# Optimization experiments

Measured on AMD Instinct MI355X. Metric: run time of the kernel, lower is better.

Reference implementation:

```python
import jax, jax.numpy as jnp
import numpy as np

B, C, T = 64, 1, 262144
NUM_BANDS = 6
# (min, max) for each of the 18 normalized control params: 6 bands x (gain_dB, cutoff_Hz, Q)
PARAM_RANGES = np.array([
    [-24.0, 24.0], [20.0, 200.0], [0.1, 10.0],      # low shelf
    [-24.0, 24.0], [200.0, 2000.0], [0.1, 10.0],    # band 1
    [-24.0, 24.0], [200.0, 2000.0], [0.1, 10.0],    # band 2
    [-24.0, 24.0], [2000.0, 8000.0], [0.1, 10.0],   # band 3
    [-24.0, 24.0], [4000.0, 12000.0], [0.1, 10.0],  # band 4
    [-24.0, 24.0], [4000.0, 12000.0], [0.1, 10.0],  # high shelf
], dtype=np.float32)
FILTER_TYPES = ["low_shelf", "peaking", "peaking", "peaking", "peaking", "high_shelf"]


def biquad_coeffs(gain_dB, cutoff, q, sr, ftype):
    # Audio-EQ-cookbook biquad coefficients; all inputs shape (B,)
    A = 10.0 ** (gain_dB / 40.0)
    w0 = 2.0 * jnp.pi * (cutoff / sr)
    alpha = jnp.sin(w0) / (2.0 * q)
    c = jnp.cos(w0)
    sA = jnp.sqrt(A)
    if ftype == "low_shelf":
        b0 = A * ((A + 1) - (A - 1) * c + 2 * sA * alpha)
        b1 = 2 * A * ((A - 1) - (A + 1) * c)
        b2 = A * ((A + 1) - (A - 1) * c - 2 * sA * alpha)
        a0 = (A + 1) + (A - 1) * c + 2 * sA * alpha
        a1 = -2 * ((A - 1) + (A + 1) * c)
        a2 = (A + 1) + (A - 1) * c - 2 * sA * alpha
    elif ftype == "high_shelf":
        b0 = A * ((A + 1) + (A - 1) * c + 2 * sA * alpha)
        b1 = -2 * A * ((A - 1) + (A + 1) * c)
        b2 = A * ((A + 1) + (A - 1) * c - 2 * sA * alpha)
        a0 = (A + 1) - (A - 1) * c + 2 * sA * alpha
        a1 = 2 * ((A - 1) - (A + 1) * c)
        a2 = (A + 1) - (A - 1) * c - 2 * sA * alpha
    else:  # peaking
        b0 = 1 + alpha * A
        b1 = -2 * c
        b2 = 1 - alpha * A
        a0 = 1 + alpha / A
        a1 = -2 * c
        a2 = 1 - alpha / A
    bcoef = jnp.stack([b0, b1, b2], axis=-1) / a0[..., None]  # (B, 3)
    acoef = jnp.stack([a0, a1, a2], axis=-1) / a0[..., None]  # (B, 3)
    return bcoef, acoef


def cascade_biquads(x, bcoefs, acoefs):
    # x: (N, T); bcoefs/acoefs: (6, N, 3). Fused cascade of 6 biquads,
    # direct form II transposed, single scan over time.
    def step(state, xt):  # state: (6, N, 2); xt: (N,)
        v = xt
        new_states = []
        for k in range(NUM_BANDS):
            bk, ak = bcoefs[k], acoefs[k]
            s1, s2 = state[k, :, 0], state[k, :, 1]
            y = bk[:, 0] * v + s1
            ns1 = bk[:, 1] * v - ak[:, 1] * y + s2
            ns2 = bk[:, 2] * v - ak[:, 2] * y
            new_states.append(jnp.stack([ns1, ns2], axis=-1))
            v = y
        return jnp.stack(new_states, axis=0), v
    init = jnp.zeros((NUM_BANDS, x.shape[0], 2), dtype=x.dtype)
    _, y = jax.lax.scan(step, init, x.T)  # y: (T, N)
    return y.T


def setup_inputs() -> dict:
    key = jax.random.key(0)
    k1, k2, k3 = jax.random.split(key, 3)
    x = jax.random.normal(k1, (B, C, T), dtype=jnp.float32) * 0.1
    p = jax.random.normal(k2, (B, 22), dtype=jnp.float32)
    W = jax.random.normal(k3, (18, 22), dtype=jnp.float32) * (1.0 / np.sqrt(22.0))
    b = jnp.zeros((18,), dtype=jnp.float32)
    return {"x": x, "p": p, "W": W, "b": b, "sample_rate": 24000}


def reference(x, p, W, b, sample_rate):
    bs, chs, s = x.shape
    sr = jnp.float32(sample_rate)
    # control path: linear + sigmoid -> 18 normalized params in [0, 1]
    pn = jax.nn.sigmoid(p @ W.T + b)  # (bs, 18)
    lo = jnp.asarray(PARAM_RANGES[:, 0])
    hi = jnp.asarray(PARAM_RANGES[:, 1])
    params = pn * (hi - lo) + lo  # denormalized, (bs, 18)
    bcoefs, acoefs = [], []
    for k, ftype in enumerate(FILTER_TYPES):
        g, f, q = params[:, 3 * k], params[:, 3 * k + 1], params[:, 3 * k + 2]
        bk, ak = biquad_coeffs(g, f, q, sr, ftype)
        bcoefs.append(bk)
        acoefs.append(ak)
    bcoefs = jnp.stack(bcoefs, axis=0)  # (6, bs, 3)
    acoefs = jnp.stack(acoefs, axis=0)
    # share each item's EQ across its channels
    bcoefs = jnp.repeat(bcoefs, chs, axis=1)  # (6, bs*chs, 3)
    acoefs = jnp.repeat(acoefs, chs, axis=1)
    y = cascade_biquads(x.reshape(bs * chs, s), bcoefs, acoefs)
    return y.reshape(bs, chs, s)
```

## Files before the change

### kernel.cpp

```cpp
#include <hip/hip_runtime.h>
#include <math.h>

#define NB    64
#define NT    262144
#define CH    64
#define NCK   (NT/CH)
#define NBANDS 6

#define COEF_OFF 0
#define MAT_OFF  4096
#define T_OFF    (MAT_OFF + NB*1728)
#define WPRE_OFF (T_OFF + NB*64*12)
#define D_OFF    (WPRE_OFF + NB*64*12)

struct Coef { float b0, b1, b2, a1, a2; };

__device__ __forceinline__ float rfl(float x) {
  return __int_as_float(__builtin_amdgcn_readfirstlane(__float_as_int(x)));
}

__device__ __forceinline__ float cascade_step(float v, float s[12], const Coef cf[NBANDS]) {
#pragma unroll
  for (int k = 0; k < NBANDS; ++k) {
    float s1 = s[2*k], s2 = s[2*k+1];
    float y   = fmaf(cf[k].b0, v, s1);
    float ns1 = fmaf(cf[k].b1, v, fmaf(-cf[k].a1, y, s2));
    float ns2 = fmaf(cf[k].b2, v, -cf[k].a2 * y);
    s[2*k]   = ns1;
    s[2*k+1] = ns2;
    v = y;
  }
  return v;
}

__device__ __forceinline__ void load_coefs(const float* ws, int batch, Coef cf[NBANDS]) {
  const float* c = ws + COEF_OFF + batch*30;
#pragma unroll
  for (int k = 0; k < NBANDS; ++k) {
    cf[k].b0 = rfl(c[5*k+0]); cf[k].b1 = rfl(c[5*k+1]); cf[k].b2 = rfl(c[5*k+2]);
    cf[k].a1 = rfl(c[5*k+3]); cf[k].a2 = rfl(c[5*k+4]);
  }
}

__global__ __launch_bounds__(64) void k_prep(const float* __restrict__ p, const float* __restrict__ W,
                                             const float* __restrict__ bias, const int* __restrict__ srp,
                                             float* __restrict__ ws) {
  __shared__ float prmS[18];
  __shared__ float cfS[30];
  __shared__ float M0[144], M1[144];
  int b = blockIdx.x, tid = threadIdx.x;
  const float lo[18] = {-24.f,20.f,0.1f,  -24.f,200.f,0.1f,  -24.f,200.f,0.1f,
                        -24.f,2000.f,0.1f, -24.f,4000.f,0.1f, -24.f,4000.f,0.1f};
  const float hi[18] = { 24.f,200.f,10.f,  24.f,2000.f,10.f,  24.f,2000.f,10.f,
                         24.f,8000.f,10.f, 24.f,12000.f,10.f, 24.f,12000.f,10.f};
  if (tid < 18) {
    float acc = bias[tid];
    for (int j = 0; j < 22; ++j) acc = fmaf(W[tid*22+j], p[b*22+j], acc);
    float sg = 1.f / (1.f + expf(-acc));
    prmS[tid] = sg * (hi[tid] - lo[tid]) + lo[tid];
  }
  __syncthreads();
  if (tid < 6) {
    int k = tid;
    float g = prmS[3*k], f = prmS[3*k+1], q = prmS[3*k+2];
    float sr = (float)srp[0];
    float A  = powf(10.f, g * (1.f/40.f));
    float w0 = 6.28318530717958647692f * (f / sr);
    float al = sinf(w0) / (2.f*q);
    float c  = cosf(w0);
    float sA = sqrtf(A);
    float b0,b1,b2,a0,a1,a2;
    if (k == 0) {
      b0 = A*((A+1.f) - (A-1.f)*c + 2.f*sA*al);
      b1 = 2.f*A*((A-1.f) - (A+1.f)*c);
      b2 = A*((A+1.f) - (A-1.f)*c - 2.f*sA*al);
      a0 = (A+1.f) + (A-1.f)*c + 2.f*sA*al;
      a1 = -2.f*((A-1.f) + (A+1.f)*c);
      a2 = (A+1.f) + (A-1.f)*c - 2.f*sA*al;
    } else if (k == 5) {
      b0 = A*((A+1.f) + (A-1.f)*c + 2.f*sA*al);
      b1 = -2.f*A*((A-1.f) + (A+1.f)*c);
      b2 = A*((A+1.f) + (A-1.f)*c - 2.f*sA*al);
      a0 = (A+1.f) - (A-1.f)*c + 2.f*sA*al;
      a1 = 2.f*((A-1.f) - (A+1.f)*c);
      a2 = (A+1.f) - (A-1.f)*c - 2.f*sA*al;
    } else {
      b0 = 1.f + al*A;
      b1 = -2.f*c;
      b2 = 1.f - al*A;
      a0 = 1.f + al/A;
      a1 = -2.f*c;
      a2 = 1.f - al/A;
    }
    float inv = 1.f/a0;
    float* cws = ws + COEF_OFF + b*30;
    cws[5*k+0] = cfS[5*k+0] = b0*inv;
    cws[5*k+1] = cfS[5*k+1] = b1*inv;
    cws[5*k+2] = cfS[5*k+2] = b2*inv;
    cws[5*k+3] = cfS[5*k+3] = a1*inv;
    cws[5*k+4] = cfS[5*k+4] = a2*inv;
  }
  __syncthreads();

  Coef cf[NBANDS];
#pragma unroll
  for (int k = 0; k < NBANDS; ++k) {
    cf[k].b0 = cfS[5*k+0]; cf[k].b1 = cfS[5*k+1]; cf[k].b2 = cfS[5*k+2];
    cf[k].a1 = cfS[5*k+3]; cf[k].a2 = cfS[5*k+4];
  }
  if (tid < 12) {
    float s[12];
#pragma unroll
    for (int r = 0; r < 12; ++r) s[r] = (r == tid) ? 1.f : 0.f;
    cascade_step(0.f, s, cf);
#pragma unroll
    for (int r = 0; r < 12; ++r) M0[r*12 + tid] = s[r];
  }
  __syncthreads();

  float w[12];
#pragma unroll
  for (int r = 0; r < 12; ++r) w[r] = 0.f;
  cascade_step(1.f, w, cf);
  int e63 = 63 - tid;

  float* S = M0; float* D = M1;
  float* mout = ws + MAT_OFF + (size_t)b*1728;
  for (int q = 0; q < 6; ++q) {
    if ((e63 >> q) & 1) {
      float t[12];
#pragma unroll
      for (int r = 0; r < 12; ++r) {
        float acc = 0.f;
#pragma unroll
        for (int k = 0; k < 12; ++k) acc = fmaf(S[r*12+k], w[k], acc);
        t[r] = acc;
      }
#pragma unroll
      for (int r = 0; r < 12; ++r) w[r] = t[r];
    }
    for (int e = tid; e < 144; e += 64) {
      int r = e/12, c = e%12;
      float acc = 0.f;
#pragma unroll
      for (int k = 0; k < 12; ++k) acc = fmaf(S[r*12+k], S[k*12+c], acc);
      D[e] = acc;
    }
    __syncthreads();
    float* t = S; S = D; D = t;
  }
  {
    float* vout = ws + WPRE_OFF + (size_t)b*768;
#pragma unroll
    for (int r = 0; r < 12; ++r) vout[tid*12 + r] = w[r];
  }
  for (int e = tid; e < 144; e += 64) mout[e] = S[e];
  for (int l = 1; l < 12; ++l) {
    for (int e = tid; e < 144; e += 64) {
      int r = e/12, c = e%12;
      float acc = 0.f;
#pragma unroll
      for (int k = 0; k < 12; ++k) acc = fmaf(S[r*12+k], S[k*12+c], acc);
      D[e] = acc;
    }
    __syncthreads();
    float* t = S; S = D; D = t;
    for (int e = tid; e < 144; e += 64) mout[l*144 + e] = S[e];
  }
}

__global__ __launch_bounds__(256) void k_passA(const float* __restrict__ x,
                                               const float* __restrict__ Vt,
                                               float* __restrict__ ws) {
  __shared__ float KM[6][144];
  int tid = threadIdx.x, wib = tid >> 6, lane = tid & 63;
  int gw = blockIdx.x*4 + wib;
  int batch = gw >> 6, wv = gw & 63;
  int batch_b = blockIdx.x >> 4;

  const float* mb = ws + MAT_OFF + (size_t)batch_b*1728;
  for (int e = tid; e < 864; e += 256) KM[e/144][e%144] = mb[e];
  __syncthreads();

  const float4* xp = (const float4*)x + (size_t)batch*65536 + (size_t)wv*1024 + (size_t)lane*16;
  const float* Vb = Vt + (size_t)batch_b*768;

  float4 xv[16];
#pragma unroll
  for (int k = 0; k < 16; ++k) xv[k] = xp[k];

  float s[12];
#pragma unroll
  for (int r = 0; r < 12; ++r) s[r] = 0.f;

#pragma unroll
  for (int k = 0; k < 16; ++k) {
    const float* vr = Vb + k*48;
#pragma unroll
    for (int r = 0; r < 12; ++r) {
      float acc = s[r];
      acc = fmaf(vr[r],      xv[k].x, acc);
      acc = fmaf(vr[12 + r], xv[k].y, acc);
      acc = fmaf(vr[24 + r], xv[k].z, acc);
      acc = fmaf(vr[36 + r], xv[k].w, acc);
      s[r] = acc;
    }
  }

#pragma unroll
  for (int l = 0; l < 6; ++l) {
    const int pd = 1 << l;
    float nb[12];
#pragma unroll
    for (int r = 0; r < 12; ++r) nb[r] = __shfl_up(s[r], pd);
    if (lane >= pd) {
#pragma unroll
      for (int r = 0; r < 12; ++r) {
        float acc = s[r];
#pragma unroll
        for (int c = 0; c < 12; ++c) acc = fmaf(KM[l][r*12+c], nb[c], acc);
        s[r] = acc;
      }
    }
  }

  if (lane == 63) {
    float4* tp = (float4*)(ws + T_OFF + ((size_t)batch*64 + wv)*12);
    tp[0] = make_float4(s[0], s[1], s[2],  s[3]);
    tp[1] = make_float4(s[4], s[5], s[6],  s[7]);
    tp[2] = make_float4(s[8], s[9], s[10], s[11]);
  }

  float e[12];
#pragma unroll
  for (int r = 0; r < 12; ++r) e[r] = __shfl_up(s[r], 1);
  if (lane == 0) {
#pragma unroll
    for (int r = 0; r < 12; ++r) e[r] = 0.f;
  }
  int chunk = wv*64 + lane;
  float4* dp = (float4*)(ws + D_OFF + ((size_t)batch*NCK + chunk)*12);
  dp[0] = make_float4(e[0], e[1], e[2],  e[3]);
  dp[1] = make_float4(e[4], e[5], e[6],  e[7]);
  dp[2] = make_float4(e[8], e[9], e[10], e[11]);
}

__global__ __launch_bounds__(64) void k_scanW(float* __restrict__ ws) {
  __shared__ float WM[6][144];
  int b = blockIdx.x, lane = threadIdx.x;
  const float* mb = ws + MAT_OFF + (size_t)b*1728 + 864;
  for (int e = lane; e < 864; e += 64) WM[e/144][e%144] = mb[e];
  __syncthreads();

  const float4* tp = (const float4*)(ws + T_OFF + ((size_t)b*64 + lane)*12);
  float4 a0 = tp[0], a1 = tp[1], a2 = tp[2];
  float s[12] = {a0.x,a0.y,a0.z,a0.w, a1.x,a1.y,a1.z,a1.w, a2.x,a2.y,a2.z,a2.w};

#pragma unroll
  for (int l = 0; l < 6; ++l) {
    const int pd = 1 << l;
    float nb[12];
#pragma unroll
    for (int r = 0; r < 12; ++r) nb[r] = __shfl_up(s[r], pd);
    if (lane >= pd) {
#pragma unroll
      for (int r = 0; r < 12; ++r) {
        float acc = s[r];
#pragma unroll
        for (int c = 0; c < 12; ++c) acc = fmaf(WM[l][r*12+c], nb[c], acc);
        s[r] = acc;
      }
    }
  }
  float e[12];
#pragma unroll
  for (int r = 0; r < 12; ++r) e[r] = __shfl_up(s[r], 1);
  if (lane == 0) {
#pragma unroll
    for (int r = 0; r < 12; ++r) e[r] = 0.f;
  }
  float4* wp = (float4*)(ws + WPRE_OFF + ((size_t)b*64 + lane)*12);
  wp[0] = make_float4(e[0], e[1], e[2],  e[3]);
  wp[1] = make_float4(e[4], e[5], e[6],  e[7]);
  wp[2] = make_float4(e[8], e[9], e[10], e[11]);
}

__global__ __launch_bounds__(256) void k_passB(const float* __restrict__ x, const float* __restrict__ ws,
                                               float* __restrict__ out) {
  __shared__ float4 buf[4][2][256];
  __shared__ float KM[6][144];
  int tid = threadIdx.x, wib = tid >> 6, lane = tid & 63;
  int gw = blockIdx.x*4 + wib;
  int batch = gw >> 6, wv = gw & 63;
  int batch_b = blockIdx.x >> 4;

  const float* mb = ws + MAT_OFF + (size_t)batch_b*1728;
  for (int e = tid; e < 864; e += 256) KM[e/144][e%144] = mb[e];
  __syncthreads();

  const float4* x4 = (const float4*)x;
  float4* out4 = (float4*)out;
  size_t gbase4 = (size_t)batch*65536 + (size_t)wv*1024;
  int r2 = lane >> 2, c2 = lane & 3;
  float4* bufA = buf[wib][0];
  float4* bufB = buf[wib][1];

  float4 va[4], vb[4];
#pragma unroll
  for (int j = 0; j < 4; ++j) va[j] = x4[gbase4 + (size_t)(j*16 + r2)*16 + c2];

  Coef cf[NBANDS];
  load_coefs(ws, batch, cf);

  int chunk = wv*64 + lane;
  const float4* dp = (const float4*)(ws + D_OFF + ((size_t)batch*NCK + chunk)*12);
  float4 e0 = dp[0], e1 = dp[1], e2 = dp[2];
  const float4* wp = (const float4*)(ws + WPRE_OFF + ((size_t)batch*64 + wv)*12);
  float4 w0 = wp[0], w1 = wp[1], w2 = wp[2];
  float R[12] = {w0.x,w0.y,w0.z,w0.w, w1.x,w1.y,w1.z,w1.w, w2.x,w2.y,w2.z,w2.w};
#pragma unroll
  for (int l = 0; l < 6; ++l) {
    float t[12];
#pragma unroll
    for (int r = 0; r < 12; ++r) {
      float acc = 0.f;
#pragma unroll
      for (int c = 0; c < 12; ++c) acc = fmaf(KM[l][r*12+c], R[c], acc);
      t[r] = acc;
    }
    bool sel = (lane >> l) & 1;
#pragma unroll
    for (int r = 0; r < 12; ++r) R[r] = sel ? t[r] : R[r];
  }
  float s[12] = {e0.x+R[0], e0.y+R[1], e0.z+R[2],  e0.w+R[3],
                 e1.x+R[4], e1.y+R[5], e1.z+R[6],  e1.w+R[7],
                 e2.x+R[8], e2.y+R[9], e2.z+R[10], e2.w+R[11]};

#pragma unroll
  for (int j = 0; j < 4; ++j) bufA[c2*64 + j*16 + r2] = va[j];
  asm volatile("s_waitcnt lgkmcnt(0)" ::: "memory");

#pragma unroll
  for (int q = 0; q < 4; ++q) {
    float4* bp = (q & 1) ? bufB : bufA;
    float4* bn = (q & 1) ? bufA : bufB;
    float4* vr = (q & 1) ? va : vb;
    if (q < 3) {
#pragma unroll
      for (int j = 0; j < 4; ++j)
        vr[j] = x4[gbase4 + (size_t)(j*16 + r2)*16 + (q+1)*4 + c2];
    }
#pragma unroll
    for (int t = 0; t < 4; ++t) {
      float4 xv = bp[t*64 + lane];
      float4 yv;
      yv.x = cascade_step(xv.x, s, cf);
      yv.y = cascade_step(xv.y, s, cf);
      yv.z = cascade_step(xv.z, s, cf);
      yv.w = cascade_step(xv.w, s, cf);
      bp[t*64 + lane] = yv;
    }
    asm volatile("s_waitcnt lgkmcnt(0)" ::: "memory");
#pragma unroll
    for (int j = 0; j < 4; ++j) {
      float4 w = bp[c2*64 + j*16 + r2];
      out4[gbase4 + (size_t)(j*16 + r2)*16 + q*4 + c2] = w;
    }
    if (q < 3) {
#pragma unroll
      for (int j = 0; j < 4; ++j) bn[c2*64 + j*16 + r2] = vr[j];
      asm volatile("s_waitcnt lgkmcnt(0)" ::: "memory");
    }
  }
}

extern "C" void kernel_launch(void* const* d_in, const int* in_sizes, int n_in,
                              void* d_out, int out_size, void* d_ws, size_t ws_size,
                              hipStream_t stream) {
  const float* x    = (const float*)d_in[0];
  const float* p    = (const float*)d_in[1];
  const float* W    = (const float*)d_in[2];
  const float* bias = (const float*)d_in[3];
  const int*   sr   = (const int*)d_in[4];
  float* ws  = (float*)d_ws;
  float* out = (float*)d_out;

  int passBlocks = (NB * NCK) / 256;
  hipLaunchKernelGGL(k_prep,  dim3(NB),         dim3(64),  0, stream, p, W, bias, sr, ws);
  hipLaunchKernelGGL(k_passA, dim3(passBlocks), dim3(256), 0, stream, x, ws + WPRE_OFF, ws);
  hipLaunchKernelGGL(k_scanW, dim3(NB),         dim3(64),  0, stream, ws);
  hipLaunchKernelGGL(k_passB, dim3(passBlocks), dim3(256), 0, stream, x, ws, out);
}
```

Measured before the change: 97.58 us.

## Recompute chunk states in replay kernel, dropping scan kernel and state buffers

Removes the separate wave-level scan kernel and the per-chunk entry-state writes to workspace. The replay kernel now recomputes the chunk projections and the intra-wave scan from the x values it holds in registers. It also redoes the 64-wave totals scan redundantly in every wave to get its prefix. This cuts one launch and a large workspace write/read round trip, at the cost of duplicated matrix-vector work and more register pressure (16 float4 held per lane, launch bounds of 4).

```diff
diff --git a/kernel.cpp b/kernel.cpp
--- a/kernel.cpp
+++ b/kernel.cpp
@@ -10,8 +10,7 @@
 #define COEF_OFF 0
 #define MAT_OFF  4096
 #define T_OFF    (MAT_OFF + NB*1728)
-#define WPRE_OFF (T_OFF + NB*64*12)
-#define D_OFF    (WPRE_OFF + NB*64*12)
+#define V_OFF    (T_OFF + NB*64*12)
 
 struct Coef { float b0, b1, b2, a1, a2; };
 
@@ -150,7 +149,7 @@
     float* t = S; S = D; D = t;
   }
   {
-    float* vout = ws + WPRE_OFF + (size_t)b*768;
+    float* vout = ws + V_OFF + (size_t)b*768;
 #pragma unroll
     for (int r = 0; r < 12; ++r) vout[tid*12 + r] = w[r];
   }
@@ -169,9 +168,8 @@
   }
 }
 
-__global__ __launch_bounds__(256) void k_passA(const float* __restrict__ x,
-                                               const float* __restrict__ Vt,
-                                               float* __restrict__ ws) {
+__global__ __launch_bounds__(256, 4) void k_totals(const float* __restrict__ x,
+                                                   float* __restrict__ ws) {
   __shared__ float KM[6][144];
   int tid = threadIdx.x, wib = tid >> 6, lane = tid & 63;
   int gw = blockIdx.x*4 + wib;
@@ -182,17 +180,17 @@
   for (int e = tid; e < 864; e += 256) KM[e/144][e%144] = mb[e];
   __syncthreads();
 
-  const float4* xp = (const float4*)x + (size_t)batch*65536 + (size_t)wv*1024 + (size_t)lane*16;
-  const float* Vb = Vt + (size_t)batch_b*768;
+  const float4* x4 = (const float4*)x;
+  size_t gbase4 = (size_t)batch*65536 + (size_t)wv*1024 + (size_t)lane*16;
+  const float* Vb = ws + V_OFF + (size_t)batch_b*768;
 
   float4 xv[16];
 #pragma unroll
-  for (int k = 0; k < 16; ++k) xv[k] = xp[k];
+  for (int k = 0; k < 16; ++k) xv[k] = x4[gbase4 + k];
 
   float s[12];
 #pragma unroll
   for (int r = 0; r < 12; ++r) s[r] = 0.f;
-
 #pragma unroll
   for (int k = 0; k < 16; ++k) {
     const float* vr = Vb + k*48;
@@ -230,94 +228,109 @@
     tp[1] = make_float4(s[4], s[5], s[6],  s[7]);
     tp[2] = make_float4(s[8], s[9], s[10], s[11]);
   }
-
-  float e[12];
-#pragma unroll
-  for (int r = 0; r < 12; ++r) e[r] = __shfl_up(s[r], 1);
-  if (lane == 0) {
-#pragma unroll
-    for (int r = 0; r < 12; ++r) e[r] = 0.f;
-  }
-  int chunk = wv*64 + lane;
-  float4* dp = (float4*)(ws + D_OFF + ((size_t)batch*NCK + chunk)*12);
-  dp[0] = make_float4(e[0], e[1], e[2],  e[3]);
-  dp[1] = make_float4(e[4], e[5], e[6],  e[7]);
-  dp[2] = make_float4(e[8], e[9], e[10], e[11]);
-}
-
-__global__ __launch_bounds__(64) void k_scanW(float* __restrict__ ws) {
-  __shared__ float WM[6][144];
-  int b = blockIdx.x, lane = threadIdx.x;
-  const float* mb = ws + MAT_OFF + (size_t)b*1728 + 864;
-  for (int e = lane; e < 864; e += 64) WM[e/144][e%144] = mb[e];
-  __syncthreads();
-
-  const float4* tp = (const float4*)(ws + T_OFF + ((size_t)b*64 + lane)*12);
-  float4 a0 = tp[0], a1 = tp[1], a2 = tp[2];
-  float s[12] = {a0.x,a0.y,a0.z,a0.w, a1.x,a1.y,a1.z,a1.w, a2.x,a2.y,a2.z,a2.w};
-
-#pragma unroll
-  for (int l = 0; l < 6; ++l) {
-    const int pd = 1 << l;
-    float nb[12];
-#pragma unroll
-    for (int r = 0; r < 12; ++r) nb[r] = __shfl_up(s[r], pd);
-    if (lane >= pd) {
-#pragma unroll
-      for (int r = 0; r < 12; ++r) {
-        float acc = s[r];
-#pragma unroll
-        for (int c = 0; c < 12; ++c) acc = fmaf(WM[l][r*12+c], nb[c], acc);
-        s[r] = acc;
-      }
-    }
-  }
-  float e[12];
-#pragma unroll
-  for (int r = 0; r < 12; ++r) e[r] = __shfl_up(s[r], 1);
-  if (lane == 0) {
-#pragma unroll
-    for (int r = 0; r < 12; ++r) e[r] = 0.f;
-  }
-  float4* wp = (float4*)(ws + WPRE_OFF + ((size_t)b*64 + lane)*12);
-  wp[0] = make_float4(e[0], e[1], e[2],  e[3]);
-  wp[1] = make_float4(e[4], e[5], e[6],  e[7]);
-  wp[2] = make_float4(e[8], e[9], e[10], e[11]);
-}
-
-__global__ __launch_bounds__(256) void k_passB(const float* __restrict__ x, const float* __restrict__ ws,
-                                               float* __restrict__ out) {
-  __shared__ float4 buf[4][2][256];
-  __shared__ float KM[6][144];
+}
+
+__global__ __launch_bounds__(256, 4) void k_replay(const float* __restrict__ x,
+                                                   const float* __restrict__ ws,
+                                                   float* __restrict__ out) {
+  __shared__ float KM[12][144];
+  __shared__ float4 sbuf[4][256];
   int tid = threadIdx.x, wib = tid >> 6, lane = tid & 63;
   int gw = blockIdx.x*4 + wib;
   int batch = gw >> 6, wv = gw & 63;
   int batch_b = blockIdx.x >> 4;
 
   const float* mb = ws + MAT_OFF + (size_t)batch_b*1728;
-  for (int e = tid; e < 864; e += 256) KM[e/144][e%144] = mb[e];
+  for (int e = tid; e < 1728; e += 256) KM[e/144][e%144] = mb[e];
+
+  Coef cf[NBANDS];
+  load_coefs(ws, batch, cf);
   __syncthreads();
 
   const float4* x4 = (const float4*)x;
   float4* out4 = (float4*)out;
-  size_t gbase4 = (size_t)batch*65536 + (size_t)wv*1024;
-  int r2 = lane >> 2, c2 = lane & 3;
-  float4* bufA = buf[wib][0];
-  float4* bufB = buf[wib][1];
-
-  float4 va[4], vb[4];
-#pragma unroll
-  for (int j = 0; j < 4; ++j) va[j] = x4[gbase4 + (size_t)(j*16 + r2)*16 + c2];
-
-  Coef cf[NBANDS];
-  load_coefs(ws, batch, cf);
-
-  int chunk = wv*64 + lane;
-  const float4* dp = (const float4*)(ws + D_OFF + ((size_t)batch*NCK + chunk)*12);
-  float4 e0 = dp[0], e1 = dp[1], e2 = dp[2];
-  const float4* wp = (const float4*)(ws + WPRE_OFF + ((size_t)batch*64 + wv)*12);
-  float4 w0 = wp[0], w1 = wp[1], w2 = wp[2];
-  float R[12] = {w0.x,w0.y,w0.z,w0.w, w1.x,w1.y,w1.z,w1.w, w2.x,w2.y,w2.z,w2.w};
+  size_t wbase4 = (size_t)batch*65536 + (size_t)wv*1024;
+  size_t gbase4 = wbase4 + (size_t)lane*16;
+  const float* Vb = ws + V_OFF + (size_t)batch_b*768;
+
+  float4 xv[16];
+#pragma unroll
+  for (int k = 0; k < 16; ++k) xv[k] = x4[gbase4 + k];
+
+  float s[12];
+#pragma unroll
+  for (int r = 0; r < 12; ++r) s[r] = 0.f;
+#pragma unroll
+  for (int k = 0; k < 16; ++k) {
+    const float* vr = Vb + k*48;
+#pragma unroll
+    for (int r = 0; r < 12; ++r) {
+      float acc = s[r];
+      acc = fmaf(vr[r],      xv[k].x, acc);
+      acc = fmaf(vr[12 + r], xv[k].y, acc);
+      acc = fmaf(vr[24 + r], xv[k].z, acc);
+      acc = fmaf(vr[36 + r], xv[k].w, acc);
+      s[r] = acc;
+    }
+  }
+
+#pragma unroll
+  for (int l = 0; l < 6; ++l) {
+    const int pd = 1 << l;
+    float nb[12];
+#pragma unroll
+    for (int r = 0; r < 12; ++r) nb[r] = __shfl_up(s[r], pd);
+    if (lane >= pd) {
+#pragma unroll
+      for (int r = 0; r < 12; ++r) {
+        float acc = s[r];
+#pragma unroll
+        for (int c = 0; c < 12; ++c) acc = fmaf(KM[l][r*12+c], nb[c], acc);
+        s[r] = acc;
+      }
+    }
+  }
+
+  float ex[12];
+#pragma unroll
+  for (int r = 0; r < 12; ++r) ex[r] = __shfl_up(s[r], 1);
+  if (lane == 0) {
+#pragma unroll
+    for (int r = 0; r < 12; ++r) ex[r] = 0.f;
+  }
+
+  const float4* tp = (const float4*)(ws + T_OFF + ((size_t)batch*64 + lane)*12);
+  float4 t0 = tp[0], t1 = tp[1], t2 = tp[2];
+  float sc[12] = {t0.x,t0.y,t0.z,t0.w, t1.x,t1.y,t1.z,t1.w, t2.x,t2.y,t2.z,t2.w};
+#pragma unroll
+  for (int l = 0; l < 6; ++l) {
+    const int pd = 1 << l;
+    float nb[12];
+#pragma unroll
+    for (int r = 0; r < 12; ++r) nb[r] = __shfl_up(sc[r], pd);
+    if (lane >= pd) {
+#pragma unroll
+      for (int r = 0; r < 12; ++r) {
+        float acc = sc[r];
+#pragma unroll
+        for (int c = 0; c < 12; ++c) acc = fmaf(KM[6+l][r*12+c], nb[c], acc);
+        sc[r] = acc;
+      }
+    }
+  }
+
+  int bsrc = (wv == 0) ? 0 : (wv - 1);
+  float pre[12];
+#pragma unroll
+  for (int r = 0; r < 12; ++r) pre[r] = __shfl(sc[r], bsrc);
+  if (wv == 0) {
+#pragma unroll
+    for (int r = 0; r < 12; ++r) pre[r] = 0.f;
+  }
+
+  float R[12];
+#pragma unroll
+  for (int r = 0; r < 12; ++r) R[r] = pre[r];
 #pragma unroll
   for (int l = 0; l < 6; ++l) {
     float t[12];
@@ -332,45 +345,32 @@
 #pragma unroll
     for (int r = 0; r < 12; ++r) R[r] = sel ? t[r] : R[r];
   }
-  float s[12] = {e0.x+R[0], e0.y+R[1], e0.z+R[2],  e0.w+R[3],
-                 e1.x+R[4], e1.y+R[5], e1.z+R[6],  e1.w+R[7],
-                 e2.x+R[8], e2.y+R[9], e2.z+R[10], e2.w+R[11]};
-
-#pragma unroll
-  for (int j = 0; j < 4; ++j) bufA[c2*64 + j*16 + r2] = va[j];
-  asm volatile("s_waitcnt lgkmcnt(0)" ::: "memory");
-
+
+  float st[12];
+#pragma unroll
+  for (int r = 0; r < 12; ++r) st[r] = ex[r] + R[r];
+
+  int r2 = lane >> 2, c2 = lane & 3;
+  float4* bp = sbuf[wib];
 #pragma unroll
   for (int q = 0; q < 4; ++q) {
-    float4* bp = (q & 1) ? bufB : bufA;
-    float4* bn = (q & 1) ? bufA : bufB;
-    float4* vr = (q & 1) ? va : vb;
-    if (q < 3) {
-#pragma unroll
-      for (int j = 0; j < 4; ++j)
-        vr[j] = x4[gbase4 + (size_t)(j*16 + r2)*16 + (q+1)*4 + c2];
-    }
 #pragma unroll
     for (int t = 0; t < 4; ++t) {
-      float4 xv = bp[t*64 + lane];
+      float4 xvv = xv[q*4 + t];
       float4 yv;
-      yv.x = cascade_step(xv.x, s, cf);
-      yv.y = cascade_step(xv.y, s, cf);
-      yv.z = cascade_step(xv.z, s, cf);
-      yv.w = cascade_step(xv.w, s, cf);
+      yv.x = cascade_step(xvv.x, st, cf);
+      yv.y = cascade_step(xvv.y, st, cf);
+      yv.z = cascade_step(xvv.z, st, cf);
+      yv.w = cascade_step(xvv.w, st, cf);
       bp[t*64 + lane] = yv;
     }
     asm volatile("s_waitcnt lgkmcnt(0)" ::: "memory");
 #pragma unroll
     for (int j = 0; j < 4; ++j) {
       float4 w = bp[c2*64 + j*16 + r2];
-      out4[gbase4 + (size_t)(j*16 + r2)*16 + q*4 + c2] = w;
-    }
-    if (q < 3) {
-#pragma unroll
-      for (int j = 0; j < 4; ++j) bn[c2*64 + j*16 + r2] = vr[j];
-      asm volatile("s_waitcnt lgkmcnt(0)" ::: "memory");
-    }
+      out4[wbase4 + (size_t)(j*16 + r2)*16 + q*4 + c2] = w;
+    }
+    asm volatile("s_waitcnt lgkmcnt(0)" ::: "memory");
   }
 }
 
@@ -386,8 +386,7 @@
   float* out = (float*)d_out;
 
   int passBlocks = (NB * NCK) / 256;
-  hipLaunchKernelGGL(k_prep,  dim3(NB),         dim3(64),  0, stream, p, W, bias, sr, ws);
-  hipLaunchKernelGGL(k_passA, dim3(passBlocks), dim3(256), 0, stream, x, ws + WPRE_OFF, ws);
-  hipLaunchKernelGGL(k_scanW, dim3(NB),         dim3(64),  0, stream, ws);
-  hipLaunchKernelGGL(k_passB, dim3(passBlocks), dim3(256), 0, stream, x, ws, out);
-}
+  hipLaunchKernelGGL(k_prep,   dim3(NB),         dim3(64),  0, stream, p, W, bias, sr, ws);
+  hipLaunchKernelGGL(k_totals, dim3(passBlocks), dim3(256), 0, stream, x, ws);
+  hipLaunchKernelGGL(k_replay, dim3(passBlocks), dim3(256), 0, stream, x, ws, out);
+}
```

Result: slower. 111.8 us (+14.6%).

## Split pass-A chunks across two half-lanes and widen the wave-level scan to 128 segments

Applied to the files above, without the earlier changes.

Pass A now has each lane reduce only 32 samples instead of 64, so two half-waves each cover 32 chunks. The halves are combined with a 32-step transition matrix, and the intra-wave scan drops to 5 levels over 32 lanes. This doubles the pass-A grid and halves per-lane register and load pressure. The grid-level scan now spans 128 segments per batch using two waves bridged through shared memory, and pass B's prefix correction uses 5 levels per 32-lane group. The cost is more workspace traffic, an extra stored matrix power, and a longer serial scanW.

```diff
diff --git a/kernel.cpp b/kernel.cpp
--- a/kernel.cpp
+++ b/kernel.cpp
@@ -9,9 +9,9 @@
 
 #define COEF_OFF 0
 #define MAT_OFF  4096
-#define T_OFF    (MAT_OFF + NB*1728)
-#define WPRE_OFF (T_OFF + NB*64*12)
-#define D_OFF    (WPRE_OFF + NB*64*12)
+#define T_OFF    (MAT_OFF + NB*1872)
+#define WPRE_OFF (T_OFF + NB*128*12)
+#define D_OFF    (WPRE_OFF + NB*128*12)
 
 struct Coef { float b0, b1, b2, a1, a2; };
 
@@ -125,7 +125,7 @@
   int e63 = 63 - tid;
 
   float* S = M0; float* D = M1;
-  float* mout = ws + MAT_OFF + (size_t)b*1728;
+  float* mout = ws + MAT_OFF + (size_t)b*1872;
   for (int q = 0; q < 6; ++q) {
     if ((e63 >> q) & 1) {
       float t[12];
@@ -139,6 +139,9 @@
 #pragma unroll
       for (int r = 0; r < 12; ++r) w[r] = t[r];
     }
+    if (q == 5) {
+      for (int e = tid; e < 144; e += 64) mout[12*144 + e] = S[e];
+    }
     for (int e = tid; e < 144; e += 64) {
       int r = e/12, c = e%12;
       float acc = 0.f;
@@ -150,7 +153,7 @@
     float* t = S; S = D; D = t;
   }
   {
-    float* vout = ws + WPRE_OFF + (size_t)b*768;
+    float* vout = ws + WPRE_OFF + (size_t)b*1536;
 #pragma unroll
     for (int r = 0; r < 12; ++r) vout[tid*12 + r] = w[r];
   }
@@ -169,133 +172,183 @@
   }
 }
 
-__global__ __launch_bounds__(256) void k_passA(const float* __restrict__ x,
-                                               const float* __restrict__ Vt,
-                                               float* __restrict__ ws) {
+__global__ __launch_bounds__(256, 8) void k_passA(const float* __restrict__ x, float* __restrict__ ws) {
   __shared__ float KM[6][144];
+  int tid = threadIdx.x, wib = tid >> 6, lane = tid & 63;
+  int gw = blockIdx.x*4 + wib;
+  int batch = gw >> 7, wv = gw & 127;
+  int batch_b = blockIdx.x >> 5;
+
+  const float* mb = ws + MAT_OFF + (size_t)batch_b*1872;
+  for (int e = tid; e < 864; e += 256) {
+    float v = (e < 720) ? mb[e] : mb[12*144 + (e - 720)];
+    KM[e/144][e%144] = v;
+  }
+  __syncthreads();
+
+  int c = lane & 31, h = lane >> 5;
+  const float4* x4 = (const float4*)x;
+  size_t gbase4 = (size_t)batch*65536 + (size_t)(wv*32 + c)*16 + (size_t)h*8;
+  const float* Vb = ws + WPRE_OFF + (size_t)batch_b*1536 + 32*12;
+
+  float4 xv[8];
+#pragma unroll
+  for (int k = 0; k < 8; ++k) xv[k] = x4[gbase4 + k];
+
+  float p[12];
+#pragma unroll
+  for (int r = 0; r < 12; ++r) p[r] = 0.f;
+#pragma unroll
+  for (int k = 0; k < 8; ++k) {
+    const float* vr = Vb + k*48;
+#pragma unroll
+    for (int r = 0; r < 12; ++r) {
+      float acc = p[r];
+      acc = fmaf(vr[r],      xv[k].x, acc);
+      acc = fmaf(vr[12 + r], xv[k].y, acc);
+      acc = fmaf(vr[24 + r], xv[k].z, acc);
+      acc = fmaf(vr[36 + r], xv[k].w, acc);
+      p[r] = acc;
+    }
+  }
+
+  float s[12];
+#pragma unroll
+  for (int r = 0; r < 12; ++r) s[r] = __shfl_down(p[r], 32);
+#pragma unroll
+  for (int r = 0; r < 12; ++r) {
+    float acc = s[r];
+#pragma unroll
+    for (int k = 0; k < 12; ++k) acc = fmaf(KM[5][r*12+k], p[k], acc);
+    s[r] = acc;
+  }
+
+#pragma unroll
+  for (int l = 0; l < 5; ++l) {
+    const int pd = 1 << l;
+    float nb[12];
+#pragma unroll
+    for (int r = 0; r < 12; ++r) nb[r] = __shfl_up(s[r], pd);
+    if (lane >= pd) {
+#pragma unroll
+      for (int r = 0; r < 12; ++r) {
+        float acc = s[r];
+#pragma unroll
+        for (int cc = 0; cc < 12; ++cc) acc = fmaf(KM[l][r*12+cc], nb[cc], acc);
+        s[r] = acc;
+      }
+    }
+  }
+
+  if (lane == 31) {
+    float4* tp = (float4*)(ws + T_OFF + ((size_t)batch*128 + wv)*12);
+    tp[0] = make_float4(s[0], s[1], s[2],  s[3]);
+    tp[1] = make_float4(s[4], s[5], s[6],  s[7]);
+    tp[2] = make_float4(s[8], s[9], s[10], s[11]);
+  }
+
+  float e[12];
+#pragma unroll
+  for (int r = 0; r < 12; ++r) e[r] = __shfl_up(s[r], 1);
+  if (lane == 0) {
+#pragma unroll
+    for (int r = 0; r < 12; ++r) e[r] = 0.f;
+  }
+  if (lane < 32) {
+    int chunk = wv*32 + lane;
+    float4* dp = (float4*)(ws + D_OFF + ((size_t)batch*NCK + chunk)*12);
+    dp[0] = make_float4(e[0], e[1], e[2],  e[3]);
+    dp[1] = make_float4(e[4], e[5], e[6],  e[7]);
+    dp[2] = make_float4(e[8], e[9], e[10], e[11]);
+  }
+}
+
+__global__ __launch_bounds__(128) void k_scanW(float* __restrict__ ws) {
+  __shared__ float WM[7][144];
+  __shared__ float bridge[12];
+  int b = blockIdx.x, t = threadIdx.x, lane = t & 63, w = t >> 6;
+  const float* mb = ws + MAT_OFF + (size_t)b*1872 + 5*144;
+  for (int e = t; e < 1008; e += 128) WM[e/144][e%144] = mb[e];
+  __syncthreads();
+
+  const float4* tp = (const float4*)(ws + T_OFF + ((size_t)b*128 + t)*12);
+  float4 a0 = tp[0], a1 = tp[1], a2 = tp[2];
+  float s[12] = {a0.x,a0.y,a0.z,a0.w, a1.x,a1.y,a1.z,a1.w, a2.x,a2.y,a2.z,a2.w};
+
+#pragma unroll
+  for (int m = 0; m < 6; ++m) {
+    const int pd = 1 << m;
+    float nb[12];
+#pragma unroll
+    for (int r = 0; r < 12; ++r) nb[r] = __shfl_up(s[r], pd);
+    if (lane >= pd) {
+#pragma unroll
+      for (int r = 0; r < 12; ++r) {
+        float acc = s[r];
+#pragma unroll
+        for (int c = 0; c < 12; ++c) acc = fmaf(WM[m][r*12+c], nb[c], acc);
+        s[r] = acc;
+      }
+    }
+  }
+  if (t == 63) {
+#pragma unroll
+    for (int r = 0; r < 12; ++r) bridge[r] = s[r];
+  }
+  __syncthreads();
+
+  if (w == 1) {
+    int k = lane + 1;
+    float R[12];
+#pragma unroll
+    for (int r = 0; r < 12; ++r) R[r] = bridge[r];
+#pragma unroll
+    for (int bit = 0; bit < 7; ++bit) {
+      if ((k >> bit) & 1) {
+        float tv[12];
+#pragma unroll
+        for (int r = 0; r < 12; ++r) {
+          float acc = 0.f;
+#pragma unroll
+          for (int c = 0; c < 12; ++c) acc = fmaf(WM[bit][r*12+c], R[c], acc);
+          tv[r] = acc;
+        }
+#pragma unroll
+        for (int r = 0; r < 12; ++r) R[r] = tv[r];
+      }
+    }
+#pragma unroll
+    for (int r = 0; r < 12; ++r) s[r] += R[r];
+  }
+
+  float e[12];
+#pragma unroll
+  for (int r = 0; r < 12; ++r) e[r] = __shfl_up(s[r], 1);
+  if (t == 0) {
+#pragma unroll
+    for (int r = 0; r < 12; ++r) e[r] = 0.f;
+  }
+  if (t == 64) {
+#pragma unroll
+    for (int r = 0; r < 12; ++r) e[r] = bridge[r];
+  }
+  float4* wp = (float4*)(ws + WPRE_OFF + ((size_t)b*128 + t)*12);
+  wp[0] = make_float4(e[0], e[1], e[2],  e[3]);
+  wp[1] = make_float4(e[4], e[5], e[6],  e[7]);
+  wp[2] = make_float4(e[8], e[9], e[10], e[11]);
+}
+
+__global__ __launch_bounds__(256) void k_passB(const float* __restrict__ x, const float* __restrict__ ws,
+                                               float* __restrict__ out) {
+  __shared__ float4 buf[4][2][256];
+  __shared__ float KM[5][144];
   int tid = threadIdx.x, wib = tid >> 6, lane = tid & 63;
   int gw = blockIdx.x*4 + wib;
   int batch = gw >> 6, wv = gw & 63;
   int batch_b = blockIdx.x >> 4;
 
-  const float* mb = ws + MAT_OFF + (size_t)batch_b*1728;
-  for (int e = tid; e < 864; e += 256) KM[e/144][e%144] = mb[e];
-  __syncthreads();
-
-  const float4* xp = (const float4*)x + (size_t)batch*65536 + (size_t)wv*1024 + (size_t)lane*16;
-  const float* Vb = Vt + (size_t)batch_b*768;
-
-  float4 xv[16];
-#pragma unroll
-  for (int k = 0; k < 16; ++k) xv[k] = xp[k];
-
-  float s[12];
-#pragma unroll
-  for (int r = 0; r < 12; ++r) s[r] = 0.f;
-
-#pragma unroll
-  for (int k = 0; k < 16; ++k) {
-    const float* vr = Vb + k*48;
-#pragma unroll
-    for (int r = 0; r < 12; ++r) {
-      float acc = s[r];
-      acc = fmaf(vr[r],      xv[k].x, acc);
-      acc = fmaf(vr[12 + r], xv[k].y, acc);
-      acc = fmaf(vr[24 + r], xv[k].z, acc);
-      acc = fmaf(vr[36 + r], xv[k].w, acc);
-      s[r] = acc;
-    }
-  }
-
-#pragma unroll
-  for (int l = 0; l < 6; ++l) {
-    const int pd = 1 << l;
-    float nb[12];
-#pragma unroll
-    for (int r = 0; r < 12; ++r) nb[r] = __shfl_up(s[r], pd);
-    if (lane >= pd) {
-#pragma unroll
-      for (int r = 0; r < 12; ++r) {
-        float acc = s[r];
-#pragma unroll
-        for (int c = 0; c < 12; ++c) acc = fmaf(KM[l][r*12+c], nb[c], acc);
-        s[r] = acc;
-      }
-    }
-  }
-
-  if (lane == 63) {
-    float4* tp = (float4*)(ws + T_OFF + ((size_t)batch*64 + wv)*12);
-    tp[0] = make_float4(s[0], s[1], s[2],  s[3]);
-    tp[1] = make_float4(s[4], s[5], s[6],  s[7]);
-    tp[2] = make_float4(s[8], s[9], s[10], s[11]);
-  }
-
-  float e[12];
-#pragma unroll
-  for (int r = 0; r < 12; ++r) e[r] = __shfl_up(s[r], 1);
-  if (lane == 0) {
-#pragma unroll
-    for (int r = 0; r < 12; ++r) e[r] = 0.f;
-  }
-  int chunk = wv*64 + lane;
-  float4* dp = (float4*)(ws + D_OFF + ((size_t)batch*NCK + chunk)*12);
-  dp[0] = make_float4(e[0], e[1], e[2],  e[3]);
-  dp[1] = make_float4(e[4], e[5], e[6],  e[7]);
-  dp[2] = make_float4(e[8], e[9], e[10], e[11]);
-}
-
-__global__ __launch_bounds__(64) void k_scanW(float* __restrict__ ws) {
-  __shared__ float WM[6][144];
-  int b = blockIdx.x, lane = threadIdx.x;
-  const float* mb = ws + MAT_OFF + (size_t)b*1728 + 864;
-  for (int e = lane; e < 864; e += 64) WM[e/144][e%144] = mb[e];
-  __syncthreads();
-
-  const float4* tp = (const float4*)(ws + T_OFF + ((size_t)b*64 + lane)*12);
-  float4 a0 = tp[0], a1 = tp[1], a2 = tp[2];
-  float s[12] = {a0.x,a0.y,a0.z,a0.w, a1.x,a1.y,a1.z,a1.w, a2.x,a2.y,a2.z,a2.w};
-
-#pragma unroll
-  for (int l = 0; l < 6; ++l) {
-    const int pd = 1 << l;
-    float nb[12];
-#pragma unroll
-    for (int r = 0; r < 12; ++r) nb[r] = __shfl_up(s[r], pd);
-    if (lane >= pd) {
-#pragma unroll
-      for (int r = 0; r < 12; ++r) {
-        float acc = s[r];
-#pragma unroll
-        for (int c = 0; c < 12; ++c) acc = fmaf(WM[l][r*12+c], nb[c], acc);
-        s[r] = acc;
-      }
-    }
-  }
-  float e[12];
-#pragma unroll
-  for (int r = 0; r < 12; ++r) e[r] = __shfl_up(s[r], 1);
-  if (lane == 0) {
-#pragma unroll
-    for (int r = 0; r < 12; ++r) e[r] = 0.f;
-  }
-  float4* wp = (float4*)(ws + WPRE_OFF + ((size_t)b*64 + lane)*12);
-  wp[0] = make_float4(e[0], e[1], e[2],  e[3]);
-  wp[1] = make_float4(e[4], e[5], e[6],  e[7]);
-  wp[2] = make_float4(e[8], e[9], e[10], e[11]);
-}
-
-__global__ __launch_bounds__(256) void k_passB(const float* __restrict__ x, const float* __restrict__ ws,
-                                               float* __restrict__ out) {
-  __shared__ float4 buf[4][2][256];
-  __shared__ float KM[6][144];
-  int tid = threadIdx.x, wib = tid >> 6, lane = tid & 63;
-  int gw = blockIdx.x*4 + wib;
-  int batch = gw >> 6, wv = gw & 63;
-  int batch_b = blockIdx.x >> 4;
-
-  const float* mb = ws + MAT_OFF + (size_t)batch_b*1728;
-  for (int e = tid; e < 864; e += 256) KM[e/144][e%144] = mb[e];
+  const float* mb = ws + MAT_OFF + (size_t)batch_b*1872;
+  for (int e = tid; e < 720; e += 256) KM[e/144][e%144] = mb[e];
   __syncthreads();
 
   const float4* x4 = (const float4*)x;
@@ -313,13 +366,14 @@
   load_coefs(ws, batch, cf);
 
   int chunk = wv*64 + lane;
+  int g = wv*2 + (lane >> 5), j = lane & 31;
   const float4* dp = (const float4*)(ws + D_OFF + ((size_t)batch*NCK + chunk)*12);
   float4 e0 = dp[0], e1 = dp[1], e2 = dp[2];
-  const float4* wp = (const float4*)(ws + WPRE_OFF + ((size_t)batch*64 + wv)*12);
+  const float4* wp = (const float4*)(ws + WPRE_OFF + ((size_t)batch*128 + g)*12);
   float4 w0 = wp[0], w1 = wp[1], w2 = wp[2];
   float R[12] = {w0.x,w0.y,w0.z,w0.w, w1.x,w1.y,w1.z,w1.w, w2.x,w2.y,w2.z,w2.w};
 #pragma unroll
-  for (int l = 0; l < 6; ++l) {
+  for (int l = 0; l < 5; ++l) {
     float t[12];
 #pragma unroll
     for (int r = 0; r < 12; ++r) {
@@ -328,7 +382,7 @@
       for (int c = 0; c < 12; ++c) acc = fmaf(KM[l][r*12+c], R[c], acc);
       t[r] = acc;
     }
-    bool sel = (lane >> l) & 1;
+    bool sel = (j >> l) & 1;
 #pragma unroll
     for (int r = 0; r < 12; ++r) R[r] = sel ? t[r] : R[r];
   }
@@ -337,7 +391,7 @@
                  e2.x+R[8], e2.y+R[9], e2.z+R[10], e2.w+R[11]};
 
 #pragma unroll
-  for (int j = 0; j < 4; ++j) bufA[c2*64 + j*16 + r2] = va[j];
+  for (int j2 = 0; j2 < 4; ++j2) bufA[c2*64 + j2*16 + r2] = va[j2];
   asm volatile("s_waitcnt lgkmcnt(0)" ::: "memory");
 
 #pragma unroll
@@ -347,8 +401,8 @@
     float4* vr = (q & 1) ? va : vb;
     if (q < 3) {
 #pragma unroll
-      for (int j = 0; j < 4; ++j)
-        vr[j] = x4[gbase4 + (size_t)(j*16 + r2)*16 + (q+1)*4 + c2];
+      for (int j2 = 0; j2 < 4; ++j2)
+        vr[j2] = x4[gbase4 + (size_t)(j2*16 + r2)*16 + (q+1)*4 + c2];
     }
 #pragma unroll
     for (int t = 0; t < 4; ++t) {
@@ -362,13 +416,13 @@
     }
     asm volatile("s_waitcnt lgkmcnt(0)" ::: "memory");
 #pragma unroll
-    for (int j = 0; j < 4; ++j) {
-      float4 w = bp[c2*64 + j*16 + r2];
-      out4[gbase4 + (size_t)(j*16 + r2)*16 + q*4 + c2] = w;
+    for (int j2 = 0; j2 < 4; ++j2) {
+      float4 w = bp[c2*64 + j2*16 + r2];
+      out4[gbase4 + (size_t)(j2*16 + r2)*16 + q*4 + c2] = w;
     }
     if (q < 3) {
 #pragma unroll
-      for (int j = 0; j < 4; ++j) bn[c2*64 + j*16 + r2] = vr[j];
+      for (int j2 = 0; j2 < 4; ++j2) bn[c2*64 + j2*16 + r2] = vr[j2];
       asm volatile("s_waitcnt lgkmcnt(0)" ::: "memory");
     }
   }
@@ -385,9 +439,8 @@
   float* ws  = (float*)d_ws;
   float* out = (float*)d_out;
 
-  int passBlocks = (NB * NCK) / 256;
-  hipLaunchKernelGGL(k_prep,  dim3(NB),         dim3(64),  0, stream, p, W, bias, sr, ws);
-  hipLaunchKernelGGL(k_passA, dim3(passBlocks), dim3(256), 0, stream, x, ws + WPRE_OFF, ws);
-  hipLaunchKernelGGL(k_scanW, dim3(NB),         dim3(64),  0, stream, ws);
-  hipLaunchKernelGGL(k_passB, dim3(passBlocks), dim3(256), 0, stream, x, ws, out);
-}
+  hipLaunchKernelGGL(k_prep,  dim3(NB),   dim3(64),  0, stream, p, W, bias, sr, ws);
+  hipLaunchKernelGGL(k_passA, dim3(2048), dim3(256), 0, stream, x, ws);
+  hipLaunchKernelGGL(k_scanW, dim3(NB),   dim3(128), 0, stream, ws);
+  hipLaunchKernelGGL(k_passB, dim3(1024), dim3(256), 0, stream, x, ws, out);
+}
```

Result: slower. 111.1 us (+13.8%).
